# Performance work log

Measured on AMD Instinct MI355X. Metric: run time of the kernel, lower is better.

Reference implementation:

```python
import jax, jax.numpy as jnp
import numpy as np
from functools import partial

B, T = 2048, 500
H1, H2, D_IN, D_FC, N_CLS = 128, 64, 1, 128, 4

def _lstm_scan(x, Wih, Whh, bih, bhh, hidden, return_seq):
    # x: (B, T, D). PyTorch gate order: i, f, g, o. Weights: (4H, D) / (4H, H).
    Bsz = x.shape[0]
    b = bih + bhh
    xg = jnp.einsum('btd,gd->btg', x, Wih) + b  # precompute input projections (B,T,4H)
    xg = jnp.swapaxes(xg, 0, 1)                 # (T,B,4H)
    h0 = jnp.zeros((Bsz, hidden), x.dtype)
    c0 = jnp.zeros((Bsz, hidden), x.dtype)

    def step(carry, gt):
        h, c = carry
        gates = gt + h @ Whh.T
        i, f, g, o = jnp.split(gates, 4, axis=-1)
        c = jax.nn.sigmoid(f) * c + jax.nn.sigmoid(i) * jnp.tanh(g)
        h = jax.nn.sigmoid(o) * jnp.tanh(c)
        return (h, c), (h if return_seq else None)

    (hT, _), hs = jax.lax.scan(step, (h0, c0), xg)
    if return_seq:
        return jnp.swapaxes(hs, 0, 1)  # (B,T,H)
    return hT  # (B,H)

def setup_inputs() -> dict:
    key = jax.random.key(0)
    ks = jax.random.split(key, 16)
    n = lambda k, shape: jax.random.normal(k, shape, dtype=jnp.float32) * 0.05
    return {
        'x': jax.random.normal(ks[0], (B, 1, T), dtype=jnp.float32),
        'Wp': n(ks[1], (H1, D_IN)), 'bp': n(ks[2], (H1,)),
        'Wih1': n(ks[3], (4 * H1, H1)), 'Whh1': n(ks[4], (4 * H1, H1)),
        'bih1': n(ks[5], (4 * H1,)), 'bhh1': n(ks[6], (4 * H1,)),
        'Wih2': n(ks[7], (4 * H2, H1)), 'Whh2': n(ks[8], (4 * H2, H2)),
        'bih2': n(ks[9], (4 * H2,)), 'bhh2': n(ks[10], (4 * H2,)),
        'W1': n(ks[11], (D_FC, H2)), 'b1': n(ks[12], (D_FC,)),
        'W2': n(ks[13], (N_CLS, D_FC)), 'b2': n(ks[14], (N_CLS,)),
    }

def reference(x, Wp, bp, Wih1, Whh1, bih1, bhh1, Wih2, Whh2, bih2, bhh2, W1, b1, W2, b2):
    # x: (B,1,T) -> (B,T,1)
    h = jnp.swapaxes(x, 1, 2)
    h = h @ Wp.T + bp                                         # (B,T,128)
    h = _lstm_scan(h, Wih1, Whh1, bih1, bhh1, H1, True)       # (B,T,128); dropout is identity in eval
    h = _lstm_scan(h, Wih2, Whh2, bih2, bhh2, H2, False)      # (B,64) == last-timestep output
    h = jax.nn.relu(h @ W1.T + b1)                            # (B,128)
    return h @ W2.T + b2                                      # (B,4)
```

## Files before the change

### kernel.cpp

```cpp
#include <hip/hip_runtime.h>


#define B_   2048
#define T_   500
#define BM   8
#define NBLK (B_ / BM)
#define NTHR 768

typedef __attribute__((ext_vector_type(8))) short bf16x8;
typedef __attribute__((ext_vector_type(4))) float f32x4;

#define LOG2E 1.44269504088896340736f

static __device__ __forceinline__ short f2bf(float f) {
  unsigned u = __builtin_bit_cast(unsigned, f);
  u = (u + 0x7fffu + ((u >> 16) & 1u)) >> 16;
  return (short)u;
}

static __device__ __forceinline__ float lstm_cell_s(float gi, float gf, float gg,
                                                    float go, float& c) {
  float Ei = __builtin_amdgcn_exp2f(-gi);
  float Eg = __builtin_amdgcn_exp2f(gg + gg);
  float Ef = __builtin_amdgcn_exp2f(-gf);
  float Eo = __builtin_amdgcn_exp2f(-go);
  float t12 = (1.f + Ei) * (1.f + Eg);
  float num = c * t12 + (Eg - 1.f) * (1.f + Ef);
  c = num * __builtin_amdgcn_rcpf((1.f + Ef) * t12);
  float Ec = __builtin_amdgcn_exp2f(2.88539008177792681472f * c);
  return (Ec - 1.f) * __builtin_amdgcn_rcpf((1.f + Eo) * (1.f + Ec));
}

__global__ __launch_bounds__(NTHR)
void lstm_fused(const float* __restrict__ X,
                const float* __restrict__ Wp,
                const float* __restrict__ bp,
                const float* __restrict__ Wih1,
                const float* __restrict__ Whh1,
                const float* __restrict__ bih1,
                const float* __restrict__ bhh1,
                const float* __restrict__ Wih2,
                const float* __restrict__ Whh2,
                const float* __restrict__ bih2,
                const float* __restrict__ bhh2,
                const float* __restrict__ W1,
                const float* __restrict__ b1,
                const float* __restrict__ W2,
                const float* __restrict__ b2,
                float* __restrict__ Out) {
  __shared__ __align__(16) short h1f[2][4][64][8];
  __shared__ __align__(16) short h2g[2][2][64][8];
  __shared__ __align__(16) short w2h[4][4][2][64][8];
  __shared__ __align__(16) float xsb[T_ * 8];
  __shared__ float h2f[8][64];

  const int tid = threadIdx.x;
  const int ln = tid & 63;
  const int wv = tid >> 6;
  const int cl = ln & 15;
  const int kg = ln >> 4;
  const int r0 = blockIdx.x * BM;
  const bool isL1 = (wv >= 4);
  const int w1 = wv - 4;

  bf16x8 Wreg[4][4];
  float uv[8];

  if (isL1) {
#pragma unroll
    for (int n = 0; n < 4; ++n) {
      const int R = n * 128 + 16 * w1 + cl;
      float u = 0.f, vv = bih1[R] + bhh1[R];
      const float4* Wi4 = (const float4*)(Wih1 + R * 128);
      const float4* Wp4 = (const float4*)Wp;
      const float4* bp4 = (const float4*)bp;
#pragma unroll 4
      for (int d = 0; d < 32; ++d) {
        float4 a = Wi4[d], pw = Wp4[d], qb = bp4[d];
        u  += a.x*pw.x + a.y*pw.y + a.z*pw.z + a.w*pw.w;
        vv += a.x*qb.x + a.y*qb.y + a.z*qb.z + a.w*qb.w;
      }
      uv[n] = u * LOG2E;
      uv[4 + n] = vv * LOG2E;
#pragma unroll
      for (int kf = 0; kf < 4; ++kf) {
        const float4* s4 = (const float4*)(Whh1 + R * 128 + kf * 32 + kg * 8);
        float4 a0 = s4[0], a1 = s4[1];
        bf16x8 fr;
        fr[0]=f2bf(a0.x*LOG2E); fr[1]=f2bf(a0.y*LOG2E);
        fr[2]=f2bf(a0.z*LOG2E); fr[3]=f2bf(a0.w*LOG2E);
        fr[4]=f2bf(a1.x*LOG2E); fr[5]=f2bf(a1.y*LOG2E);
        fr[6]=f2bf(a1.z*LOG2E); fr[7]=f2bf(a1.w*LOG2E);
        Wreg[n][kf] = fr;
      }
    }
  } else {
#pragma unroll
    for (int n = 0; n < 4; ++n) {
      const int R = n * 64 + 16 * wv + cl;
      uv[n] = (bih2[R] + bhh2[R]) * LOG2E;
#pragma unroll
      for (int kf = 0; kf < 4; ++kf) {
        const float4* s4 = (const float4*)(Wih2 + R * 128 + kf * 32 + kg * 8);
        float4 a0 = s4[0], a1 = s4[1];
        bf16x8 fr;
        fr[0]=f2bf(a0.x*LOG2E); fr[1]=f2bf(a0.y*LOG2E);
        fr[2]=f2bf(a0.z*LOG2E); fr[3]=f2bf(a0.w*LOG2E);
        fr[4]=f2bf(a1.x*LOG2E); fr[5]=f2bf(a1.y*LOG2E);
        fr[6]=f2bf(a1.z*LOG2E); fr[7]=f2bf(a1.w*LOG2E);
        Wreg[n][kf] = fr;
      }
#pragma unroll
      for (int kf = 0; kf < 2; ++kf) {
        const float4* s4 = (const float4*)(Whh2 + R * 64 + kf * 32 + kg * 8);
        float4 a0 = s4[0], a1 = s4[1];
        short* dst = &w2h[wv][n][kf][ln][0];
        dst[0]=f2bf(a0.x*LOG2E); dst[1]=f2bf(a0.y*LOG2E);
        dst[2]=f2bf(a0.z*LOG2E); dst[3]=f2bf(a0.w*LOG2E);
        dst[4]=f2bf(a1.x*LOG2E); dst[5]=f2bf(a1.y*LOG2E);
        dst[6]=f2bf(a1.z*LOG2E); dst[7]=f2bf(a1.w*LOG2E);
      }
    }
  }

  for (int i = tid; i < 2 * 4 * 64 * 8; i += NTHR) ((short*)h1f)[i] = 0;
  for (int i = tid; i < 2 * 2 * 64 * 8; i += NTHR) ((short*)h2g)[i] = 0;
#pragma unroll
  for (int r = 0; r < 8; ++r)
    for (int t = tid; t < T_; t += NTHR)
      xsb[t * 8 + r] = X[(size_t)(r0 + r) * T_ + t];
  __syncthreads();

  float c0 = 0.f, c1 = 0.f;
  const int rA = (kg < 2) ? kg * 4 : (kg - 2) * 4 + 2;
  const int rB = rA + 1;
  const int uu = 16 * (isL1 ? w1 : wv) + cl;
  const int wkf = uu >> 5, wg = ((uu >> 3) & 3) * 16, wel = uu & 7;
  const float xmask = (kg < 2) ? 1.f : 0.f;

#define L1_STEP(i, cur, prv)                                                  \
  {                                                                           \
    bf16x8 a1[4];                                                             \
    _Pragma("unroll")                                                         \
    for (int kf = 0; kf < 4; ++kf)                                            \
      a1[kf] = *(const bf16x8*)&h1f[prv][kf][ln][0];                          \
    f32x4 xr4 = *(const f32x4*)&xsb[(i) * 8 + (kg & 1) * 4];                  \
    _Pragma("unroll")                                                         \
    for (int e = 0; e < 4; ++e) xr4[e] *= xmask;                              \
    f32x4 acc[4];                                                             \
    _Pragma("unroll")                                                         \
    for (int n = 0; n < 4; ++n) {                                             \
      _Pragma("unroll")                                                       \
      for (int e = 0; e < 4; ++e)                                             \
        acc[n][e] = xr4[e] * uv[n] + uv[4 + n];                               \
    }                                                                         \
    __builtin_amdgcn_s_setprio(1);                                            \
    _Pragma("unroll")                                                         \
    for (int n = 0; n < 4; ++n)                                               \
      _Pragma("unroll")                                                       \
      for (int kf = 0; kf < 4; ++kf)                                          \
        acc[n] = __builtin_amdgcn_mfma_f32_16x16x32_bf16(                     \
            a1[kf], Wreg[n][kf], acc[n], 0, 0, 0);                            \
    __builtin_amdgcn_s_setprio(0);                                            \
    float gA[4], gB[4];                                                       \
    _Pragma("unroll")                                                         \
    for (int n = 0; n < 4; ++n) {                                             \
      float s2 = __shfl_xor(acc[n][2], 32);                                   \
      float s3 = __shfl_xor(acc[n][3], 32);                                   \
      gA[n] = (kg < 2) ? acc[n][0] : s2;                                      \
      gB[n] = (kg < 2) ? acc[n][1] : s3;                                      \
    }                                                                         \
    float hA = lstm_cell_s(gA[0], gA[1], gA[2], gA[3], c0);                   \
    float hB = lstm_cell_s(gB[0], gB[1], gB[2], gB[3], c1);                   \
    unsigned pk;                                                              \
    asm("v_cvt_pk_bf16_f32 %0, %1, %2" : "=v"(pk) : "v"(hA), "v"(hB));        \
    h1f[cur][wkf][wg + rA][wel] = (short)pk;                                  \
    h1f[cur][wkf][wg + rB][wel] = (short)(pk >> 16);                          \
  }

#define L2_STEP(cur, prv, FINAL)                                              \
  {                                                                           \
    bf16x8 a1[4], ag[2];                                                      \
    _Pragma("unroll")                                                         \
    for (int kf = 0; kf < 4; ++kf)                                            \
      a1[kf] = *(const bf16x8*)&h1f[prv][kf][ln][0];                          \
    _Pragma("unroll")                                                         \
    for (int kf = 0; kf < 2; ++kf)                                            \
      ag[kf] = *(const bf16x8*)&h2g[cur][kf][ln][0];                          \
    f32x4 acc[4];                                                             \
    _Pragma("unroll")                                                         \
    for (int n = 0; n < 4; ++n)                                               \
      acc[n] = (f32x4){uv[n], uv[n], uv[n], uv[n]};                           \
    __builtin_amdgcn_s_setprio(1);                                            \
    _Pragma("unroll")                                                         \
    for (int n = 0; n < 4; ++n) {                                             \
      bf16x8 w0 = *(const bf16x8*)&w2h[wv][n][0][ln][0];                      \
      bf16x8 w1f = *(const bf16x8*)&w2h[wv][n][1][ln][0];                     \
      acc[n] = __builtin_amdgcn_mfma_f32_16x16x32_bf16(ag[0], w0,             \
                                                       acc[n], 0, 0, 0);      \
      acc[n] = __builtin_amdgcn_mfma_f32_16x16x32_bf16(ag[1], w1f,            \
                                                       acc[n], 0, 0, 0);      \
      _Pragma("unroll")                                                       \
      for (int kf = 0; kf < 4; ++kf)                                          \
        acc[n] = __builtin_amdgcn_mfma_f32_16x16x32_bf16(                     \
            a1[kf], Wreg[n][kf], acc[n], 0, 0, 0);                            \
    }                                                                         \
    __builtin_amdgcn_s_setprio(0);                                            \
    float gA[4], gB[4];                                                       \
    _Pragma("unroll")                                                         \
    for (int n = 0; n < 4; ++n) {                                             \
      float s2 = __shfl_xor(acc[n][2], 32);                                   \
      float s3 = __shfl_xor(acc[n][3], 32);                                   \
      gA[n] = (kg < 2) ? acc[n][0] : s2;                                      \
      gB[n] = (kg < 2) ? acc[n][1] : s3;                                      \
    }                                                                         \
    float hA = lstm_cell_s(gA[0], gA[1], gA[2], gA[3], c0);                   \
    float hB = lstm_cell_s(gB[0], gB[1], gB[2], gB[3], c1);                   \
    unsigned pk;                                                              \
    asm("v_cvt_pk_bf16_f32 %0, %1, %2" : "=v"(pk) : "v"(hA), "v"(hB));        \
    h2g[prv][wkf][wg + rA][wel] = (short)pk;                                  \
    h2g[prv][wkf][wg + rB][wel] = (short)(pk >> 16);                          \
    if (FINAL) { h2f[rA][uu] = hA; h2f[rB][uu] = hB; }                        \
  }

  if (isL1) L1_STEP(0, 0, 1);
  __syncthreads();

  for (int i = 1; i < T_; ++i) {
    const int cur = i & 1, prv = cur ^ 1;
    if (isL1) {
      L1_STEP(i, cur, prv);
    } else {
      L2_STEP(cur, prv, 0);
    }
    __syncthreads();
  }

  if (!isL1) L2_STEP(0, 1, 1);
  __syncthreads();

  float* fc1s = xsb;
  if (tid < 512) {
    const int u = tid & 127, r2 = tid >> 7;
    float a0 = b1[u], a1f = b1[u];
    for (int k = 0; k < 64; ++k) {
      float w = W1[u * 64 + k];
      a0  += h2f[r2 * 2 + 0][k] * w;
      a1f += h2f[r2 * 2 + 1][k] * w;
    }
    fc1s[(r2 * 2 + 0) * 132 + u] = fmaxf(a0, 0.f);
    fc1s[(r2 * 2 + 1) * 132 + u] = fmaxf(a1f, 0.f);
  }
  __syncthreads();
  if (tid < 32) {
    const int r = tid >> 2, cls = tid & 3;
    float a = b2[cls];
    for (int k = 0; k < 128; ++k) a += fc1s[r * 132 + k] * W2[cls * 128 + k];
    Out[(size_t)(r0 + r) * 4 + cls] = a;
  }
}

extern "C" void kernel_launch(void* const* d_in, const int* in_sizes, int n_in,
                              void* d_out, int out_size, void* d_ws, size_t ws_size,
                              hipStream_t stream) {
  const float* X    = (const float*)d_in[0];
  const float* Wp   = (const float*)d_in[1];
  const float* bp   = (const float*)d_in[2];
  const float* Wih1 = (const float*)d_in[3];
  const float* Whh1 = (const float*)d_in[4];
  const float* bih1 = (const float*)d_in[5];
  const float* bhh1 = (const float*)d_in[6];
  const float* Wih2 = (const float*)d_in[7];
  const float* Whh2 = (const float*)d_in[8];
  const float* bih2 = (const float*)d_in[9];
  const float* bhh2 = (const float*)d_in[10];
  const float* W1   = (const float*)d_in[11];
  const float* b1   = (const float*)d_in[12];
  const float* W2   = (const float*)d_in[13];
  const float* b2   = (const float*)d_in[14];
  float* Out = (float*)d_out;

  hipLaunchKernelGGL(lstm_fused, dim3(NBLK), dim3(NTHR), 0, stream,
                     X, Wp, bp, Wih1, Whh1, bih1, bhh1,
                     Wih2, Whh2, bih2, bhh2, W1, b1, W2, b2, Out);
}
```

Baseline: 511.4 us.

## Halve batch rows per block to double block count and occupancy

Reduces the batch tile per workgroup from 8 rows to 4, doubling the number of workgroups so more CUs run the recurrent chain in parallel. Each lane now computes one LSTM cell instead of two, which needs an extra cross-lane shuffle to move gate values into place. The MFMA tiles stay 16 wide, so the row padding is larger and per-row MFMA efficiency drops. With 256 blocks before, this uses more of the machine's CUs and shortens the per-step elementwise tail.

```diff
diff --git a/kernel.cpp b/kernel.cpp
--- a/kernel.cpp
+++ b/kernel.cpp
@@ -3,7 +3,7 @@
 
 #define B_   2048
 #define T_   500
-#define BM   8
+#define BM   4
 #define NBLK (B_ / BM)
 #define NTHR 768
 
@@ -51,8 +51,8 @@
   __shared__ __align__(16) short h1f[2][4][64][8];
   __shared__ __align__(16) short h2g[2][2][64][8];
   __shared__ __align__(16) short w2h[4][4][2][64][8];
-  __shared__ __align__(16) float xsb[T_ * 8];
-  __shared__ float h2f[8][64];
+  __shared__ __align__(16) float xsb[T_ * 4];
+  __shared__ float h2f[4][64];
 
   const int tid = threadIdx.x;
   const int ln = tid & 63;
@@ -126,17 +126,25 @@
   for (int i = tid; i < 2 * 4 * 64 * 8; i += NTHR) ((short*)h1f)[i] = 0;
   for (int i = tid; i < 2 * 2 * 64 * 8; i += NTHR) ((short*)h2g)[i] = 0;
 #pragma unroll
-  for (int r = 0; r < 8; ++r)
+  for (int r = 0; r < 4; ++r)
     for (int t = tid; t < T_; t += NTHR)
-      xsb[t * 8 + r] = X[(size_t)(r0 + r) * T_ + t];
-  __syncthreads();
-
-  float c0 = 0.f, c1 = 0.f;
-  const int rA = (kg < 2) ? kg * 4 : (kg - 2) * 4 + 2;
-  const int rB = rA + 1;
+      xsb[t * 4 + r] = X[(size_t)(r0 + r) * T_ + t];
+  __syncthreads();
+
+  float c0 = 0.f;
   const int uu = 16 * (isL1 ? w1 : wv) + cl;
   const int wkf = uu >> 5, wg = ((uu >> 3) & 3) * 16, wel = uu & 7;
-  const float xmask = (kg < 2) ? 1.f : 0.f;
+  const float xmask = (kg == 0) ? 1.f : 0.f;
+
+#define REDIST(accn, g)                                                       \
+  {                                                                           \
+    float s2 = __shfl_xor(accn[2], 32);                                       \
+    float s3 = __shfl_xor(accn[3], 32);                                       \
+    float pA = (kg < 2) ? accn[0] : s2;                                       \
+    float pB = (kg < 2) ? accn[1] : s3;                                       \
+    float t16 = __shfl_xor(pB, 16);                                           \
+    g = ((kg & 1) == 0) ? pA : t16;                                           \
+  }
 
 #define L1_STEP(i, cur, prv)                                                  \
   {                                                                           \
@@ -144,7 +152,7 @@
     _Pragma("unroll")                                                         \
     for (int kf = 0; kf < 4; ++kf)                                            \
       a1[kf] = *(const bf16x8*)&h1f[prv][kf][ln][0];                          \
-    f32x4 xr4 = *(const f32x4*)&xsb[(i) * 8 + (kg & 1) * 4];                  \
+    f32x4 xr4 = *(const f32x4*)&xsb[(i) * 4];                                 \
     _Pragma("unroll")                                                         \
     for (int e = 0; e < 4; ++e) xr4[e] *= xmask;                              \
     f32x4 acc[4];                                                             \
@@ -162,20 +170,13 @@
         acc[n] = __builtin_amdgcn_mfma_f32_16x16x32_bf16(                     \
             a1[kf], Wreg[n][kf], acc[n], 0, 0, 0);                            \
     __builtin_amdgcn_s_setprio(0);                                            \
-    float gA[4], gB[4];                                                       \
-    _Pragma("unroll")                                                         \
-    for (int n = 0; n < 4; ++n) {                                             \
-      float s2 = __shfl_xor(acc[n][2], 32);                                   \
-      float s3 = __shfl_xor(acc[n][3], 32);                                   \
-      gA[n] = (kg < 2) ? acc[n][0] : s2;                                      \
-      gB[n] = (kg < 2) ? acc[n][1] : s3;                                      \
-    }                                                                         \
-    float hA = lstm_cell_s(gA[0], gA[1], gA[2], gA[3], c0);                   \
-    float hB = lstm_cell_s(gB[0], gB[1], gB[2], gB[3], c1);                   \
+    float g0, g1, g2, g3;                                                     \
+    REDIST(acc[0], g0); REDIST(acc[1], g1);                                   \
+    REDIST(acc[2], g2); REDIST(acc[3], g3);                                   \
+    float h = lstm_cell_s(g0, g1, g2, g3, c0);                                \
     unsigned pk;                                                              \
-    asm("v_cvt_pk_bf16_f32 %0, %1, %2" : "=v"(pk) : "v"(hA), "v"(hB));        \
-    h1f[cur][wkf][wg + rA][wel] = (short)pk;                                  \
-    h1f[cur][wkf][wg + rB][wel] = (short)(pk >> 16);                          \
+    asm("v_cvt_pk_bf16_f32 %0, %1, %2" : "=v"(pk) : "v"(h), "v"(h));          \
+    h1f[cur][wkf][wg + kg][wel] = (short)pk;                                  \
   }
 
 #define L2_STEP(cur, prv, FINAL)                                              \
@@ -206,21 +207,14 @@
             a1[kf], Wreg[n][kf], acc[n], 0, 0, 0);                            \
     }                                                                         \
     __builtin_amdgcn_s_setprio(0);                                            \
-    float gA[4], gB[4];                                                       \
-    _Pragma("unroll")                                                         \
-    for (int n = 0; n < 4; ++n) {                                             \
-      float s2 = __shfl_xor(acc[n][2], 32);                                   \
-      float s3 = __shfl_xor(acc[n][3], 32);                                   \
-      gA[n] = (kg < 2) ? acc[n][0] : s2;                                      \
-      gB[n] = (kg < 2) ? acc[n][1] : s3;                                      \
-    }                                                                         \
-    float hA = lstm_cell_s(gA[0], gA[1], gA[2], gA[3], c0);                   \
-    float hB = lstm_cell_s(gB[0], gB[1], gB[2], gB[3], c1);                   \
+    float g0, g1, g2, g3;                                                     \
+    REDIST(acc[0], g0); REDIST(acc[1], g1);                                   \
+    REDIST(acc[2], g2); REDIST(acc[3], g3);                                   \
+    float h = lstm_cell_s(g0, g1, g2, g3, c0);                                \
     unsigned pk;                                                              \
-    asm("v_cvt_pk_bf16_f32 %0, %1, %2" : "=v"(pk) : "v"(hA), "v"(hB));        \
-    h2g[prv][wkf][wg + rA][wel] = (short)pk;                                  \
-    h2g[prv][wkf][wg + rB][wel] = (short)(pk >> 16);                          \
-    if (FINAL) { h2f[rA][uu] = hA; h2f[rB][uu] = hB; }                        \
+    asm("v_cvt_pk_bf16_f32 %0, %1, %2" : "=v"(pk) : "v"(h), "v"(h));          \
+    h2g[prv][wkf][wg + kg][wel] = (short)pk;                                  \
+    if (FINAL) h2f[kg][uu] = h;                                               \
   }
 
   if (isL1) L1_STEP(0, 0, 1);
@@ -242,17 +236,13 @@
   float* fc1s = xsb;
   if (tid < 512) {
     const int u = tid & 127, r2 = tid >> 7;
-    float a0 = b1[u], a1f = b1[u];
-    for (int k = 0; k < 64; ++k) {
-      float w = W1[u * 64 + k];
-      a0  += h2f[r2 * 2 + 0][k] * w;
-      a1f += h2f[r2 * 2 + 1][k] * w;
-    }
-    fc1s[(r2 * 2 + 0) * 132 + u] = fmaxf(a0, 0.f);
-    fc1s[(r2 * 2 + 1) * 132 + u] = fmaxf(a1f, 0.f);
-  }
-  __syncthreads();
-  if (tid < 32) {
+    float a0 = b1[u];
+    for (int k = 0; k < 64; ++k)
+      a0 += h2f[r2][k] * W1[u * 64 + k];
+    fc1s[r2 * 132 + u] = fmaxf(a0, 0.f);
+  }
+  __syncthreads();
+  if (tid < 16) {
     const int r = tid >> 2, cls = tid & 3;
     float a = b2[cls];
     for (int k = 0; k < 128; ++k) a += fc1s[r * 132 + k] * W2[cls * 128 + k];
```

Result: slower. 1.014 ms (+98.3%).
